# Performance work log

Hardware: AMD Instinct MI355X
Metric: run time of the kernel (lower is better)

## Reference

```python
import jax, jax.numpy as jnp
import numpy as np

N_HEAD = 12

def _rotate_half(x):
    # interleaved rotation: (-x1, x0, -x3, x2, ...)
    x_even = x[..., ::2]
    x_odd = x[..., 1::2]
    return jnp.stack((-x_odd, x_even), axis=-1).reshape(x.shape)

def _rope_tables(T, D, dtype):
    inv_freq = 1.0 / (10000.0 ** (jnp.arange(0, D, 2, dtype=jnp.float32) / D))
    freqs = jnp.arange(T, dtype=jnp.float32)[:, None] * inv_freq[None, :]  # [T, D/2]
    cos = jnp.repeat(jnp.cos(freqs), 2, axis=-1).astype(dtype)  # [T, D]
    sin = jnp.repeat(jnp.sin(freqs), 2, axis=-1).astype(dtype)
    return cos, sin

def setup_inputs() -> dict:
    key = jax.random.key(0)
    ks = jax.random.split(key, 5)
    B, T, C = 8, 1024, 768
    return {
        "x": jax.random.normal(ks[0], (B, T, C), dtype=jnp.float32),
        "W_attn": jax.random.normal(ks[1], (C, 3 * C), dtype=jnp.float32) * (C ** -0.5),
        "b_attn": jax.random.normal(ks[2], (3 * C,), dtype=jnp.float32) * 0.02,
        "W_proj": jax.random.normal(ks[3], (C, C), dtype=jnp.float32) * (C ** -0.5),
        "b_proj": jax.random.normal(ks[4], (C,), dtype=jnp.float32) * 0.02,
    }

def reference(x, W_attn, b_attn, W_proj, b_proj):
    B, T, C = x.shape
    H = N_HEAD
    D = C // H
    qkv = x @ W_attn + b_attn  # [B, T, 3C]
    q, k, v = jnp.split(qkv, 3, axis=-1)
    # [B, H, T, D]
    q = q.reshape(B, T, H, D).transpose(0, 2, 1, 3)
    k = k.reshape(B, T, H, D).transpose(0, 2, 1, 3)
    v = v.reshape(B, T, H, D).transpose(0, 2, 1, 3)
    cos, sin = _rope_tables(T, D, x.dtype)  # [T, D]
    q = q * cos + _rotate_half(q) * sin
    k = k * cos + _rotate_half(k) * sin
    att = jnp.einsum('bhqd,bhkd->bhqk', q, k) * (D ** -0.5)
    causal = jnp.tril(jnp.ones((T, T), dtype=bool))
    att = jnp.where(causal, att, -jnp.inf)
    att = jax.nn.softmax(att, axis=-1)
    y = jnp.einsum('bhqk,bhkd->bhqd', att, v)  # [B, H, T, D]
    y = y.transpose(0, 2, 1, 3).reshape(B, T, C)
    return y @ W_proj + b_proj
```

## Files before the change

kernel.cpp:

```cpp
#include <hip/hip_runtime.h>
#include <hip/hip_bf16.h>
#include <cstdint>
#include <cstddef>

typedef __attribute__((ext_vector_type(8))) short frag8;
typedef __attribute__((ext_vector_type(4))) float facc4;

__device__ __forceinline__ float b2f(unsigned short u) {
  union { unsigned int i; float f; } v; v.i = ((unsigned int)u) << 16; return v.f;
}
__device__ __forceinline__ unsigned short f2b(float f) {
  union { float f; unsigned int i; } v; v.f = f;
  unsigned int u = v.i;
  unsigned int r = (u + 0x7fffu + ((u >> 16) & 1u)) >> 16;
  return (unsigned short)r;
}
__device__ __forceinline__ unsigned long long pk4(float a, float b, float c, float d) {
  union { __hip_bfloat162 h2[2]; unsigned long long u; } pk;
  pk.h2[0] = __float22bfloat162_rn(float2{a, b});
  pk.h2[1] = __float22bfloat162_rn(float2{c, d});
  return pk.u;
}


__global__ void cvt_f32_bf16_k(const float* __restrict__ in, unsigned short* __restrict__ out, int n8) {
  int i = blockIdx.x * blockDim.x + threadIdx.x;
  if (i >= n8) return;
  const float4* p = (const float4*)in + (size_t)i * 2;
  float4 a = p[0], b = p[1];
  union { unsigned short u[8]; frag8 v; } o;
  o.u[0] = f2b(a.x); o.u[1] = f2b(a.y); o.u[2] = f2b(a.z); o.u[3] = f2b(a.w);
  o.u[4] = f2b(b.x); o.u[5] = f2b(b.y); o.u[6] = f2b(b.z); o.u[7] = f2b(b.w);
  *((frag8*)out + i) = o.v;
}

__global__ void transpose_cvt_k(const float* __restrict__ W, unsigned short* __restrict__ Wt, int R, int Cn) {
  __shared__ float tile[32][33];
  int tx = threadIdx.x, ty = threadIdx.y;
  int c = blockIdx.x * 32 + tx;
  #pragma unroll
  for (int i = 0; i < 32; i += 8)
    tile[ty + i][tx] = W[(size_t)(blockIdx.y * 32 + ty + i) * Cn + c];
  __syncthreads();
  int rr = blockIdx.y * 32 + tx;
  #pragma unroll
  for (int i = 0; i < 32; i += 8)
    Wt[(size_t)(blockIdx.x * 32 + ty + i) * R + rr] = f2b(tile[tx][ty + i]);
}

__global__ void rope_tables_k(float* __restrict__ cosT, float* __restrict__ sinT) {
  int id = blockIdx.x * 256 + threadIdx.x;
  int t = id >> 5, i = id & 31;
  float freq = powf(10000.0f, -(float)i * (1.0f / 32.0f));
  float a = (float)t * freq;
  cosT[id] = cosf(a);
  sinT[id] = sinf(a);
}

__global__ void rope_k(unsigned short* __restrict__ Q, unsigned short* __restrict__ Kb,
                       const float* __restrict__ cosT, const float* __restrict__ sinT) {
  int id = blockIdx.x * 256 + threadIdx.x;
  int i = id & 31;
  int t = (id >> 5) & 1023;
  int bh = id >> 15;
  size_t base = ((size_t)bh << 16) + (size_t)t * 64 + i * 2;
  float c = cosT[(t << 5) + i], s = sinT[(t << 5) + i];
  unsigned int* qp = (unsigned int*)(Q + base);
  unsigned int qu = *qp;
  float q0 = b2f(qu & 0xffffu), q1 = b2f(qu >> 16);
  *qp = (unsigned int)f2b(q0 * c - q1 * s) | ((unsigned int)f2b(q1 * c + q0 * s) << 16);
  unsigned int* kp = (unsigned int*)(Kb + base);
  unsigned int ku = *kp;
  float k0 = b2f(ku & 0xffffu), k1 = b2f(ku >> 16);
  *kp = (unsigned int)f2b(k0 * c - k1 * s) | ((unsigned int)f2b(k1 * c + k0 * s) << 16);
}


#define GLDK 72

template<int EPI>
__global__ __launch_bounds__(256)
void gemm128_k(const unsigned short* __restrict__ A, const unsigned short* __restrict__ Bt,
               const float* __restrict__ bias, float* __restrict__ outF,
               unsigned short* __restrict__ Qo, unsigned short* __restrict__ Ko,
               unsigned short* __restrict__ Vo, int M, int N, int K)
{
  __shared__ unsigned short As[128 * GLDK];
  __shared__ unsigned short Bs[128 * GLDK];
  const int tid = threadIdx.x;
  const int lane = tid & 63;
  const int w = tid >> 6, wm = w >> 1, wn = w & 1;
  const int g = lane >> 4, cL = lane & 15;

  const int nwg = gridDim.x * gridDim.y;
  const int flat = blockIdx.y * gridDim.x + blockIdx.x;
  const int cpx = nwg >> 3;
  const int swz = (flat & 7) * cpx + (flat >> 3);
  const int tM = (swz / gridDim.x) * 128, tN = (swz % gridDim.x) * 128;

  facc4 zero4 = {0.f, 0.f, 0.f, 0.f};
  facc4 acc[4][4];
  #pragma unroll
  for (int i = 0; i < 4; ++i)
    #pragma unroll
    for (int j = 0; j < 4; ++j) acc[i][j] = zero4;

  const int sr = tid >> 3;
  const int sc = (tid & 7) * 8;

  for (int k0 = 0; k0 < K; k0 += 64) {
    #pragma unroll
    for (int ch = 0; ch < 4; ++ch) {
      int r = sr + ch * 32;
      frag8 va = *(const frag8*)(A  + (size_t)(tM + r) * K + k0 + sc);
      frag8 vb = *(const frag8*)(Bt + (size_t)(tN + r) * K + k0 + sc);
      *(frag8*)(&As[r * GLDK + sc]) = va;
      *(frag8*)(&Bs[r * GLDK + sc]) = vb;
    }
    __syncthreads();
    #pragma unroll
    for (int kk = 0; kk < 2; ++kk) {
      frag8 af[4], bfr[4];
      #pragma unroll
      for (int i = 0; i < 4; ++i)
        af[i] = *(const frag8*)(&As[(wm * 64 + i * 16 + cL) * GLDK + kk * 32 + g * 8]);
      #pragma unroll
      for (int j = 0; j < 4; ++j)
        bfr[j] = *(const frag8*)(&Bs[(wn * 64 + j * 16 + cL) * GLDK + kk * 32 + g * 8]);
      #pragma unroll
      for (int i = 0; i < 4; ++i)
        #pragma unroll
        for (int j = 0; j < 4; ++j)
          acc[i][j] = __builtin_amdgcn_mfma_f32_16x16x32_bf16(af[i], bfr[j], acc[i][j], 0, 0, 0);
    }
    __syncthreads();
  }

  #pragma unroll
  for (int i = 0; i < 4; ++i) {
    #pragma unroll
    for (int j = 0; j < 4; ++j) {
      const int col = tN + wn * 64 + j * 16 + cL;
      const float bv = bias[col];
      if constexpr (EPI == 0) {
        const int sel = col / 768;
        const int cc = col - sel * 768;
        const int h = cc >> 6, d = cc & 63;
        #pragma unroll
        for (int r = 0; r < 4; ++r) {
          const int m = tM + wm * 64 + i * 16 + g * 4 + r;
          const float v = acc[i][j][r] + bv;
          const int b = m >> 10, t = m & 1023;
          const size_t hb = ((size_t)(b * 12 + h)) << 16;
          if (sel == 0)      Qo[hb + (size_t)t * 64 + d] = f2b(v * 0.125f);
          else if (sel == 1) Ko[hb + (size_t)t * 64 + d] = f2b(v);
          else               Vo[hb + ((size_t)d << 10) + t] = f2b(v);
        }
      } else {
        #pragma unroll
        for (int r = 0; r < 4; ++r) {
          const int m = tM + wm * 64 + i * 16 + g * 4 + r;
          outF[(size_t)m * N + col] = acc[i][j][r] + bv;
        }
      }
    }
  }
}


__global__ __launch_bounds__(256, 4)
void attn_k(const unsigned short* __restrict__ Q, const unsigned short* __restrict__ Kb,
            const unsigned short* __restrict__ Vt, unsigned short* __restrict__ Y)
{
  __shared__ unsigned short Pl[4 * 16 * GLDK];
  const int tid = threadIdx.x, lane = tid & 63, w = tid >> 6;
  const int g = lane >> 4, cL = lane & 15;

  const int bid = blockIdx.x;
  const int xcd = bid & 7;
  const int slot = bid >> 3;
  const int bh = xcd + 8 * (slot % 12);
  const int qb = 15 - slot / 12;
  const int qw = qb * 64 + w * 16;
  const size_t hb = ((size_t)bh) << 16;

  frag8 qf[2];
  #pragma unroll
  for (int ks = 0; ks < 2; ++ks)
    qf[ks] = *(const frag8*)(Q + hb + (size_t)(qw + cL) * 64 + ks * 32 + g * 8);

  const unsigned short* Kp = Kb + hb + (size_t)cL * 64 + g * 8;
  const unsigned short* Vp = Vt + hb + (size_t)cL * 1024 + g * 8;
  unsigned short* PlW = &Pl[w * (16 * GLDK)];

  facc4 zero4 = {0.f, 0.f, 0.f, 0.f};
  facc4 o[4];
  #pragma unroll
  for (int jd = 0; jd < 4; ++jd) o[jd] = zero4;
  float mrow = -1e30f, lrow = 0.f;

  const int ntiles = qb + 1;
  for (int it = 0; it < ntiles; ++it) {
    const int kv0 = it * 64;
    frag8 kf[2][4];
    #pragma unroll
    for (int ks = 0; ks < 2; ++ks)
      #pragma unroll
      for (int j = 0; j < 4; ++j)
        kf[ks][j] = *(const frag8*)(Kp + (size_t)(kv0 + j * 16) * 64 + ks * 32);
    facc4 s[4];
    #pragma unroll
    for (int j = 0; j < 4; ++j) s[j] = zero4;
    #pragma unroll
    for (int ks = 0; ks < 2; ++ks)
      #pragma unroll
      for (int j = 0; j < 4; ++j)
        s[j] = __builtin_amdgcn_mfma_f32_16x16x32_bf16(kf[ks][j], qf[ks], s[j], 0, 0, 0);
    frag8 vf[2][4];
    #pragma unroll
    for (int ks = 0; ks < 2; ++ks)
      #pragma unroll
      for (int jd = 0; jd < 4; ++jd)
        vf[ks][jd] = *(const frag8*)(Vp + (size_t)(jd * 16) * 1024 + kv0 + ks * 32);

    if (kv0 + 63 > qw) {
      const int qrow = qw + cL;
      #pragma unroll
      for (int j = 0; j < 4; ++j)
        #pragma unroll
        for (int r = 0; r < 4; ++r)
          if (kv0 + j * 16 + g * 4 + r > qrow) s[j][r] = -1e30f;
    }
    float pm = fmaxf(fmaxf(fmaxf(s[0][0], s[0][1]), fmaxf(s[0][2], s[0][3])),
                     fmaxf(fmaxf(s[1][0], s[1][1]), fmaxf(s[1][2], s[1][3])));
    pm = fmaxf(pm, fmaxf(fmaxf(fmaxf(s[2][0], s[2][1]), fmaxf(s[2][2], s[2][3])),
                         fmaxf(fmaxf(s[3][0], s[3][1]), fmaxf(s[3][2], s[3][3]))));
    pm = fmaxf(pm, __shfl_xor(pm, 16));
    pm = fmaxf(pm, __shfl_xor(pm, 32));

    const float mn = fmaxf(mrow, pm);
    const float sc_ = __expf(mrow - mn);
    mrow = mn;
    float rs = 0.f;
    #pragma unroll
    for (int j = 0; j < 4; ++j)
      #pragma unroll
      for (int r = 0; r < 4; ++r) {
        const float p = __expf(s[j][r] - mn);
        s[j][r] = p;
        rs += p;
      }
    #pragma unroll
    for (int j = 0; j < 4; ++j)
      *(unsigned long long*)(&PlW[cL * GLDK + j * 16 + g * 4]) =
          pk4(s[j][0], s[j][1], s[j][2], s[j][3]);
    rs += __shfl_xor(rs, 16);
    rs += __shfl_xor(rs, 32);
    lrow = lrow * sc_ + rs;
    #pragma unroll
    for (int jd = 0; jd < 4; ++jd)
      #pragma unroll
      for (int r = 0; r < 4; ++r)
        o[jd][r] *= sc_;
    #pragma unroll
    for (int ks = 0; ks < 2; ++ks) {
      frag8 pa = *(const frag8*)(&PlW[cL * GLDK + ks * 32 + g * 8]);
      #pragma unroll
      for (int jd = 0; jd < 4; ++jd)
        o[jd] = __builtin_amdgcn_mfma_f32_16x16x32_bf16(vf[ks][jd], pa, o[jd], 0, 0, 0);
    }
  }

  const int b = bh / 12, h = bh - (bh / 12) * 12;
  const float inv = 1.0f / lrow;
  const size_t yrow = (size_t)(b * 1024 + qw + cL) * 768 + h * 64;
  #pragma unroll
  for (int jd = 0; jd < 4; ++jd)
    *(unsigned long long*)(&Y[yrow + jd * 16 + g * 4]) =
        pk4(o[jd][0] * inv, o[jd][1] * inv, o[jd][2] * inv, o[jd][3] * inv);
}


extern "C" void kernel_launch(void* const* d_in, const int* in_sizes, int n_in,
                              void* d_out, int out_size, void* d_ws, size_t ws_size,
                              hipStream_t stream) {
  const float* x      = (const float*)d_in[0];
  const float* W_attn = (const float*)d_in[1];
  const float* b_attn = (const float*)d_in[2];
  const float* W_proj = (const float*)d_in[3];
  const float* b_proj = (const float*)d_in[4];
  float* out = (float*)d_out;
  char* ws = (char*)d_ws;

  unsigned short* xb  = (unsigned short*)(ws);
  unsigned short* WtA = (unsigned short*)(ws + 12582912);
  unsigned short* WtP = (unsigned short*)(ws + 16121856);
  unsigned short* Qb  = (unsigned short*)(ws + 17301504);
  unsigned short* Kb  = (unsigned short*)(ws + 29884416);
  unsigned short* Vt  = (unsigned short*)(ws + 42467328);
  unsigned short* Yb  = (unsigned short*)(ws + 55050240);
  float* cosT = (float*)(ws + 67633152);
  float* sinT = (float*)(ws + 67764224);

  cvt_f32_bf16_k<<<3072, 256, 0, stream>>>(x, xb, 786432);
  transpose_cvt_k<<<dim3(72, 24), dim3(32, 8), 0, stream>>>(W_attn, WtA, 768, 2304);
  transpose_cvt_k<<<dim3(24, 24), dim3(32, 8), 0, stream>>>(W_proj, WtP, 768, 768);
  rope_tables_k<<<128, 256, 0, stream>>>(cosT, sinT);
  gemm128_k<0><<<dim3(18, 64), 256, 0, stream>>>(xb, WtA, b_attn, nullptr, Qb, Kb, Vt, 8192, 2304, 768);
  rope_k<<<12288, 256, 0, stream>>>(Qb, Kb, cosT, sinT);
  attn_k<<<1536, 256, 0, stream>>>(Qb, Kb, Vt, Yb);
  gemm128_k<1><<<dim3(6, 64), 256, 0, stream>>>(Yb, WtP, b_proj, out, nullptr, nullptr, nullptr, 8192, 768, 768);
}
```

Measured before the change: 291.0 us.

## Pair complementary causal query tiles per block to share K/V loads

```diff
diff --git a/kernel.cpp b/kernel.cpp
--- a/kernel.cpp
+++ b/kernel.cpp
@@ -168,11 +168,53 @@
 }
 
 
-__global__ __launch_bounds__(256, 4)
+__device__ __forceinline__ void sm_pv(facc4 (&s)[4], frag8 (&vf)[2][4],
+                                      unsigned short* PlW, int g, int cL,
+                                      float& m, float& l, facc4 (&o)[4]) {
+  float pm = fmaxf(fmaxf(fmaxf(s[0][0], s[0][1]), fmaxf(s[0][2], s[0][3])),
+                   fmaxf(fmaxf(s[1][0], s[1][1]), fmaxf(s[1][2], s[1][3])));
+  pm = fmaxf(pm, fmaxf(fmaxf(fmaxf(s[2][0], s[2][1]), fmaxf(s[2][2], s[2][3])),
+                       fmaxf(fmaxf(s[3][0], s[3][1]), fmaxf(s[3][2], s[3][3]))));
+  pm = fmaxf(pm, __shfl_xor(pm, 16));
+  pm = fmaxf(pm, __shfl_xor(pm, 32));
+  const float mn = fmaxf(m, pm);
+  const float sc_ = __expf(m - mn);
+  m = mn;
+  float rs = 0.f;
+  #pragma unroll
+  for (int j = 0; j < 4; ++j)
+    #pragma unroll
+    for (int r = 0; r < 4; ++r) {
+      const float p = __expf(s[j][r] - mn);
+      s[j][r] = p;
+      rs += p;
+    }
+  #pragma unroll
+  for (int j = 0; j < 4; ++j)
+    *(unsigned long long*)(&PlW[cL * GLDK + j * 16 + g * 4]) =
+        pk4(s[j][0], s[j][1], s[j][2], s[j][3]);
+  rs += __shfl_xor(rs, 16);
+  rs += __shfl_xor(rs, 32);
+  l = l * sc_ + rs;
+  #pragma unroll
+  for (int jd = 0; jd < 4; ++jd)
+    #pragma unroll
+    for (int r = 0; r < 4; ++r)
+      o[jd][r] *= sc_;
+  #pragma unroll
+  for (int ks = 0; ks < 2; ++ks) {
+    frag8 pa = *(const frag8*)(&PlW[cL * GLDK + ks * 32 + g * 8]);
+    #pragma unroll
+    for (int jd = 0; jd < 4; ++jd)
+      o[jd] = __builtin_amdgcn_mfma_f32_16x16x32_bf16(vf[ks][jd], pa, o[jd], 0, 0, 0);
+  }
+}
+
+__global__ __launch_bounds__(256, 3)
 void attn_k(const unsigned short* __restrict__ Q, const unsigned short* __restrict__ Kb,
             const unsigned short* __restrict__ Vt, unsigned short* __restrict__ Y)
 {
-  __shared__ unsigned short Pl[4 * 16 * GLDK];
+  __shared__ unsigned short Pl[8 * 16 * GLDK];
   const int tid = threadIdx.x, lane = tid & 63, w = tid >> 6;
   const int g = lane >> 4, cL = lane & 15;
 
@@ -180,104 +222,102 @@
   const int xcd = bid & 7;
   const int slot = bid >> 3;
   const int bh = xcd + 8 * (slot % 12);
-  const int qb = 15 - slot / 12;
-  const int qw = qb * 64 + w * 16;
+  const int x = slot / 12;
+  const int qwA = (15 - x) * 64 + w * 16;
+  const int qwB = x * 64 + w * 16;
+  const int ntA = 16 - x, ntB = x + 1;
   const size_t hb = ((size_t)bh) << 16;
 
-  frag8 qf[2];
-  #pragma unroll
-  for (int ks = 0; ks < 2; ++ks)
-    qf[ks] = *(const frag8*)(Q + hb + (size_t)(qw + cL) * 64 + ks * 32 + g * 8);
+  frag8 qfA[2], qfB[2];
+  #pragma unroll
+  for (int ks = 0; ks < 2; ++ks) {
+    qfA[ks] = *(const frag8*)(Q + hb + (size_t)(qwA + cL) * 64 + ks * 32 + g * 8);
+    qfB[ks] = *(const frag8*)(Q + hb + (size_t)(qwB + cL) * 64 + ks * 32 + g * 8);
+  }
 
   const unsigned short* Kp = Kb + hb + (size_t)cL * 64 + g * 8;
   const unsigned short* Vp = Vt + hb + (size_t)cL * 1024 + g * 8;
-  unsigned short* PlW = &Pl[w * (16 * GLDK)];
+  unsigned short* PlA = &Pl[w * (16 * GLDK)];
+  unsigned short* PlB = &Pl[(4 + w) * (16 * GLDK)];
 
   facc4 zero4 = {0.f, 0.f, 0.f, 0.f};
-  facc4 o[4];
-  #pragma unroll
-  for (int jd = 0; jd < 4; ++jd) o[jd] = zero4;
-  float mrow = -1e30f, lrow = 0.f;
-
-  const int ntiles = qb + 1;
-  for (int it = 0; it < ntiles; ++it) {
+  facc4 oA[4], oB[4];
+  #pragma unroll
+  for (int jd = 0; jd < 4; ++jd) { oA[jd] = zero4; oB[jd] = zero4; }
+  float mA = -1e30f, lA = 0.f, mB = -1e30f, lB = 0.f;
+
+  frag8 kf[2][4];
+  #pragma unroll
+  for (int ks = 0; ks < 2; ++ks)
+    #pragma unroll
+    for (int j = 0; j < 4; ++j)
+      kf[ks][j] = *(const frag8*)(Kp + (size_t)(j * 16) * 64 + ks * 32);
+
+  for (int it = 0; it < ntA; ++it) {
     const int kv0 = it * 64;
-    frag8 kf[2][4];
+    const bool doB = (it < ntB);
+    facc4 sA[4], sB[4];
+    #pragma unroll
+    for (int j = 0; j < 4; ++j) { sA[j] = zero4; sB[j] = zero4; }
     #pragma unroll
     for (int ks = 0; ks < 2; ++ks)
       #pragma unroll
       for (int j = 0; j < 4; ++j)
-        kf[ks][j] = *(const frag8*)(Kp + (size_t)(kv0 + j * 16) * 64 + ks * 32);
-    facc4 s[4];
-    #pragma unroll
-    for (int j = 0; j < 4; ++j) s[j] = zero4;
-    #pragma unroll
-    for (int ks = 0; ks < 2; ++ks)
-      #pragma unroll
-      for (int j = 0; j < 4; ++j)
-        s[j] = __builtin_amdgcn_mfma_f32_16x16x32_bf16(kf[ks][j], qf[ks], s[j], 0, 0, 0);
+        sA[j] = __builtin_amdgcn_mfma_f32_16x16x32_bf16(kf[ks][j], qfA[ks], sA[j], 0, 0, 0);
+    if (doB) {
+      #pragma unroll
+      for (int ks = 0; ks < 2; ++ks)
+        #pragma unroll
+        for (int j = 0; j < 4; ++j)
+          sB[j] = __builtin_amdgcn_mfma_f32_16x16x32_bf16(kf[ks][j], qfB[ks], sB[j], 0, 0, 0);
+    }
     frag8 vf[2][4];
     #pragma unroll
     for (int ks = 0; ks < 2; ++ks)
       #pragma unroll
       for (int jd = 0; jd < 4; ++jd)
         vf[ks][jd] = *(const frag8*)(Vp + (size_t)(jd * 16) * 1024 + kv0 + ks * 32);
-
-    if (kv0 + 63 > qw) {
-      const int qrow = qw + cL;
+    if (it + 1 < ntA) {
+      const int kn = (it + 1) * 64;
+      #pragma unroll
+      for (int ks = 0; ks < 2; ++ks)
+        #pragma unroll
+        for (int j = 0; j < 4; ++j)
+          kf[ks][j] = *(const frag8*)(Kp + (size_t)(kn + j * 16) * 64 + ks * 32);
+    }
+    if (kv0 + 63 > qwA) {
+      const int qrow = qwA + cL;
       #pragma unroll
       for (int j = 0; j < 4; ++j)
         #pragma unroll
         for (int r = 0; r < 4; ++r)
-          if (kv0 + j * 16 + g * 4 + r > qrow) s[j][r] = -1e30f;
-    }
-    float pm = fmaxf(fmaxf(fmaxf(s[0][0], s[0][1]), fmaxf(s[0][2], s[0][3])),
-                     fmaxf(fmaxf(s[1][0], s[1][1]), fmaxf(s[1][2], s[1][3])));
-    pm = fmaxf(pm, fmaxf(fmaxf(fmaxf(s[2][0], s[2][1]), fmaxf(s[2][2], s[2][3])),
-                         fmaxf(fmaxf(s[3][0], s[3][1]), fmaxf(s[3][2], s[3][3]))));
-    pm = fmaxf(pm, __shfl_xor(pm, 16));
-    pm = fmaxf(pm, __shfl_xor(pm, 32));
-
-    const float mn = fmaxf(mrow, pm);
-    const float sc_ = __expf(mrow - mn);
-    mrow = mn;
-    float rs = 0.f;
-    #pragma unroll
-    for (int j = 0; j < 4; ++j)
-      #pragma unroll
-      for (int r = 0; r < 4; ++r) {
-        const float p = __expf(s[j][r] - mn);
-        s[j][r] = p;
-        rs += p;
-      }
-    #pragma unroll
-    for (int j = 0; j < 4; ++j)
-      *(unsigned long long*)(&PlW[cL * GLDK + j * 16 + g * 4]) =
-          pk4(s[j][0], s[j][1], s[j][2], s[j][3]);
-    rs += __shfl_xor(rs, 16);
-    rs += __shfl_xor(rs, 32);
-    lrow = lrow * sc_ + rs;
-    #pragma unroll
-    for (int jd = 0; jd < 4; ++jd)
-      #pragma unroll
-      for (int r = 0; r < 4; ++r)
-        o[jd][r] *= sc_;
-    #pragma unroll
-    for (int ks = 0; ks < 2; ++ks) {
-      frag8 pa = *(const frag8*)(&PlW[cL * GLDK + ks * 32 + g * 8]);
-      #pragma unroll
-      for (int jd = 0; jd < 4; ++jd)
-        o[jd] = __builtin_amdgcn_mfma_f32_16x16x32_bf16(vf[ks][jd], pa, o[jd], 0, 0, 0);
-    }
+          if (kv0 + j * 16 + g * 4 + r > qrow) sA[j][r] = -1e30f;
+    }
+    if (doB && kv0 + 63 > qwB) {
+      const int qrow = qwB + cL;
+      #pragma unroll
+      for (int j = 0; j < 4; ++j)
+        #pragma unroll
+        for (int r = 0; r < 4; ++r)
+          if (kv0 + j * 16 + g * 4 + r > qrow) sB[j][r] = -1e30f;
+    }
+    sm_pv(sA, vf, PlA, g, cL, mA, lA, oA);
+    if (doB) sm_pv(sB, vf, PlB, g, cL, mB, lB, oB);
   }
 
   const int b = bh / 12, h = bh - (bh / 12) * 12;
-  const float inv = 1.0f / lrow;
-  const size_t yrow = (size_t)(b * 1024 + qw + cL) * 768 + h * 64;
+  const float invA = 1.0f / lA;
+  const size_t yrowA = (size_t)(b * 1024 + qwA + cL) * 768 + h * 64;
   #pragma unroll
   for (int jd = 0; jd < 4; ++jd)
-    *(unsigned long long*)(&Y[yrow + jd * 16 + g * 4]) =
-        pk4(o[jd][0] * inv, o[jd][1] * inv, o[jd][2] * inv, o[jd][3] * inv);
+    *(unsigned long long*)(&Y[yrowA + jd * 16 + g * 4]) =
+        pk4(oA[jd][0] * invA, oA[jd][1] * invA, oA[jd][2] * invA, oA[jd][3] * invA);
+  const float invB = 1.0f / lB;
+  const size_t yrowB = (size_t)(b * 1024 + qwB + cL) * 768 + h * 64;
+  #pragma unroll
+  for (int jd = 0; jd < 4; ++jd)
+    *(unsigned long long*)(&Y[yrowB + jd * 16 + g * 4]) =
+        pk4(oB[jd][0] * invB, oB[jd][1] * invB, oB[jd][2] * invB, oB[jd][3] * invB);
 }
 
 
@@ -308,6 +348,6 @@
   rope_tables_k<<<128, 256, 0, stream>>>(cosT, sinT);
   gemm128_k<0><<<dim3(18, 64), 256, 0, stream>>>(xb, WtA, b_attn, nullptr, Qb, Kb, Vt, 8192, 2304, 768);
   rope_k<<<12288, 256, 0, stream>>>(Qb, Kb, cosT, sinT);
-  attn_k<<<1536, 256, 0, stream>>>(Qb, Kb, Vt, Yb);
+  attn_k<<<768, 256, 0, stream>>>(Qb, Kb, Vt, Yb);
   gemm128_k<1><<<dim3(6, 64), 256, 0, stream>>>(Yb, WtP, b_proj, out, nullptr, nullptr, nullptr, 8192, 768, 768);
 }
```

After: 281.6 us. 1.03x faster.
